# Optimization experiments

Measured on AMD Instinct MI355X. Metric: run time of the kernel, lower is better.

## Reference

```python
import jax, jax.numpy as jnp
import numpy as np

T_NUM = 1024      # tracks
DET_NUM = 1024    # detections
DEG = 64          # candidate detections per track
E = T_NUM * DEG   # directed track->det edges (row<col half)
N = T_NUM + DET_NUM
D_IN = 512
D_EMB = 256
LAM = 5.0
SLACK = -0.2
SINKHORN_ITERS = 8


def setup_inputs() -> dict:
    key = jax.random.key(0)
    ks = jax.random.split(key, 20)
    x = jax.random.normal(ks[0], (N, D_IN), jnp.float32)
    coords = jax.random.uniform(ks[1], (N, 4), dtype=jnp.float32)
    r = jax.random.uniform(ks[2], (N, 4), dtype=jnp.float32)
    bx1 = r[:, 0] * 100.0; by1 = r[:, 1] * 100.0
    bw = r[:, 2] * 50.0 + 1.0; bh = r[:, 3] * 50.0 + 1.0
    coords_original = jnp.stack([bx1, by1, bx1 + bw, by1 + bh], axis=1)
    src_t = jnp.repeat(jnp.arange(T_NUM, dtype=jnp.int32), DEG)
    off = jnp.tile(jnp.arange(DEG, dtype=jnp.int32), T_NUM)
    dst_d = (src_t * 13 + off) % DET_NUM            # unique det per (track, slot)
    src = src_t
    dst = dst_d + T_NUM                              # detection node ids come after tracks
    edge_index = jnp.concatenate([jnp.stack([src, dst]), jnp.stack([dst, src])], axis=1)
    ground_truth = jax.random.bernoulli(ks[3], 0.1, (T_NUM * DET_NUM,)).astype(jnp.float32)

    def lin(k, i, o):
        return jax.random.normal(k, (i, o), jnp.float32) / np.sqrt(i).astype(np.float32)

    params = {
        'W_enc': lin(ks[4], D_IN, D_EMB), 'b_enc': jnp.zeros((D_EMB,), jnp.float32),
        'W1a': lin(ks[5], 2 * D_EMB, 64), 'b1a': jnp.zeros((64,), jnp.float32),
        'W2a': lin(ks[6], 64, 1), 'b2a': jnp.zeros((1,), jnp.float32),
        'W1g': lin(ks[7], 8, 16), 'b1g': jnp.zeros((16,), jnp.float32),
        'W2g': lin(ks[8], 16, 1), 'b2g': jnp.zeros((1,), jnp.float32),
        'W1f': lin(ks[9], 2, 8), 'b1f': jnp.zeros((8,), jnp.float32),
        'W2f': lin(ks[10], 8, 1), 'b2f': jnp.zeros((1,), jnp.float32),
        'Wn': lin(ks[11], D_EMB, D_EMB), 'Wm': lin(ks[12], D_EMB, D_EMB),
        'bo': jnp.zeros((D_EMB,), jnp.float32),
        'W1c': lin(ks[13], 2, 8), 'b1c': jnp.zeros((8,), jnp.float32),
        'W2c': lin(ks[14], 8, 1), 'b2c': jnp.zeros((1,), jnp.float32),
    }
    out = {'x': x, 'coords': coords, 'coords_original': coords_original,
           'ground_truth': ground_truth, 'edge_index': edge_index}
    out.update(params)
    return out


def _box_iou(a, b):
    # a, b: [E, 4] boxes (x1, y1, x2, y2)
    lt = jnp.maximum(a[:, :2], b[:, :2])
    rb = jnp.minimum(a[:, 2:], b[:, 2:])
    wh = jnp.clip(rb - lt, 0.0)
    inter = wh[:, 0] * wh[:, 1]
    area_a = (a[:, 2] - a[:, 0]) * (a[:, 3] - a[:, 1])
    area_b = (b[:, 2] - b[:, 0]) * (b[:, 3] - b[:, 1])
    return inter / (area_a + area_b - inter + 1e-9)


def _sinkhorn(M):
    def body(M, _):
        M = M / (jnp.sum(M, axis=1, keepdims=True) + 1e-9)
        M = M / (jnp.sum(M, axis=0, keepdims=True) + 1e-9)
        return M, None
    M, _ = jax.lax.scan(body, M, None, length=SINKHORN_ITERS)
    return M


def _forward(x, coords, coords_original,
             W_enc, b_enc, W1a, b1a, W2a, b2a, W1g, b1g, W2g, b2g,
             W1f, b1f, W2f, b2f, Wn, Wm, bo, W1c, b1c, W2c, b2c,
             edge_index):
    node = jax.nn.relu(x @ W_enc + b_enc)                      # [N, D_EMB]
    src, dst = edge_index[0], edge_index[1]                    # [2E]
    # batched per-edge appearance affinity (replaces python edge loop)
    pair = jnp.concatenate([node[src], node[dst]], axis=1)     # [2E, 2*D_EMB]
    a1 = jax.nn.relu(pair @ W1a + b1a) @ W2a + b2a             # [2E, 1]
    geo = jnp.concatenate([coords[src], coords[dst]], axis=1)  # [2E, 8]
    a2 = jax.nn.relu(geo @ W1g + b1g) @ W2g + b2g              # [2E, 1]
    e_in = jnp.concatenate([a1, a2], axis=1)                   # [2E, 2]
    edge_emb = jax.nn.relu(e_in @ W1f + b1f) @ W2f + b2f       # [2E, 1]
    # optim_net: one round of edge-weighted message passing
    msg = jax.ops.segment_sum(edge_emb * node[src], dst, num_segments=N)
    out = jax.nn.relu(node @ Wn + msg @ Wm + bo)               # [N, D_EMB]
    # forward (row < col) edges are the first E entries by construction
    sf, df = src[:E], dst[:E]
    oa, ob = out[sf], out[df]
    denom = jnp.maximum(jnp.linalg.norm(oa, axis=1) * jnp.linalg.norm(ob, axis=1), 1e-6)
    cosv = jnp.sum(oa * ob, axis=1) / denom                    # CosineSimilarity(dim=0) per edge
    iou = _box_iou(coords_original[sf], coords_original[df])   # [E]
    f_in = jnp.stack([cosv, iou], axis=1)                      # [E, 2]
    aff = (jax.nn.relu(f_in @ W1c + b1c) @ W2c + b2c)[:, 0]    # [E]
    # assignment matrix with slack row/col, scatter exp(aff*lam)
    slack_val = jnp.exp(jnp.float32(SLACK * LAM))
    M = jnp.full((T_NUM + 1, DET_NUM + 1), slack_val, jnp.float32)
    M = M.at[:T_NUM, :DET_NUM].set(0.0)
    M = M.at[sf, df - T_NUM].set(jnp.exp(aff * LAM))
    M = _sinkhorn(M)
    return M[:-1, :-1].reshape(-1)                             # [T_NUM*DET_NUM]


def reference(x, coords, coords_original, ground_truth, edge_index,
              W_enc, b_enc, W1a, b1a, W2a, b2a, W1g, b1g, W2g, b2g,
              W1f, b1f, W2f, b2f, Wn, Wm, bo, W1c, b1c, W2c, b2c):
    normalized_output = _forward(x, coords, coords_original,
                                 W_enc, b_enc, W1a, b1a, W2a, b2a,
                                 W1g, b1g, W2g, b2g, W1f, b1f, W2f, b2f,
                                 Wn, Wm, bo, W1c, b1c, W2c, b2c, edge_index)
    det_num = jnp.asarray(DET_NUM, jnp.int32)
    tracklet_num = jnp.asarray(T_NUM, jnp.int32)
    return (normalized_output, ground_truth, det_num, tracklet_num)
```

## Files before the change

kernel.cpp:

```cpp
#include <hip/hip_runtime.h>

#define T_NUM 1024
#define DET_NUM 1024
#define E_NUM 65536
#define TWO_E 131072
#define N_NODES 2048
#define D_IN 512
#define D_EMB 256

__device__ __forceinline__ unsigned bf16r(float x) {
  const unsigned u = __float_as_uint(x);
  return (u + 0x7fffu + ((u >> 16) & 1u)) >> 16;
}
__device__ __forceinline__ float bflo(unsigned p) { return __uint_as_float(p << 16); }
__device__ __forceinline__ float bfhi(unsigned p) { return __uint_as_float(p & 0xffff0000u); }

__global__ __launch_bounds__(256) void k_enc_pg(
    const float* __restrict__ x, const float* __restrict__ W,
    const float* __restrict__ b, const float* __restrict__ coords,
    const float* __restrict__ W1a, const float* __restrict__ W1g,
    float* __restrict__ node, float* __restrict__ P1, float* __restrict__ P2,
    float* __restrict__ G1, float* __restrict__ G2) {
  __shared__ __align__(16) float ns[4][D_EMB];
  const int j = threadIdx.x;
  const int row0 = blockIdx.x * 4;
  float acc[4];
  const float bj = b[j];
#pragma unroll
  for (int r = 0; r < 4; r++) acc[r] = bj;
  const float* xr = x + (size_t)row0 * D_IN;
  for (int k = 0; k < D_IN; k += 4) {
    const float w0 = W[(k + 0) * D_EMB + j];
    const float w1 = W[(k + 1) * D_EMB + j];
    const float w2 = W[(k + 2) * D_EMB + j];
    const float w3 = W[(k + 3) * D_EMB + j];
#pragma unroll
    for (int r = 0; r < 4; r++) {
      const float4 xv = *reinterpret_cast<const float4*>(xr + (size_t)r * D_IN + k);
      acc[r] = fmaf(xv.x, w0, acc[r]);
      acc[r] = fmaf(xv.y, w1, acc[r]);
      acc[r] = fmaf(xv.z, w2, acc[r]);
      acc[r] = fmaf(xv.w, w3, acc[r]);
    }
  }
#pragma unroll
  for (int r = 0; r < 4; r++) {
    const float v = fmaxf(acc[r], 0.f);
    node[(size_t)(row0 + r) * D_EMB + j] = v;
    ns[r][j] = v;
  }
  __syncthreads();
  {
    const int r = j >> 6, h = j & 63;
    float a1 = 0.f, a2 = 0.f;
    for (int k = 0; k < D_EMB; k += 4) {
      const float4 nv = *reinterpret_cast<const float4*>(&ns[r][k]);
      a1 = fmaf(nv.x, W1a[(k + 0) * 64 + h], a1);
      a1 = fmaf(nv.y, W1a[(k + 1) * 64 + h], a1);
      a1 = fmaf(nv.z, W1a[(k + 2) * 64 + h], a1);
      a1 = fmaf(nv.w, W1a[(k + 3) * 64 + h], a1);
      a2 = fmaf(nv.x, W1a[(D_EMB + k + 0) * 64 + h], a2);
      a2 = fmaf(nv.y, W1a[(D_EMB + k + 1) * 64 + h], a2);
      a2 = fmaf(nv.z, W1a[(D_EMB + k + 2) * 64 + h], a2);
      a2 = fmaf(nv.w, W1a[(D_EMB + k + 3) * 64 + h], a2);
    }
    P1[(size_t)(row0 + r) * 64 + h] = a1;
    P2[(size_t)(row0 + r) * 64 + h] = a2;
  }
  if (j < 64) {
    const int r = j >> 4, h = j & 15;
    const int n = row0 + r;
    float g1 = 0.f, g2 = 0.f;
#pragma unroll
    for (int k = 0; k < 4; k++) {
      const float c = coords[(size_t)n * 4 + k];
      g1 = fmaf(c, W1g[k * 16 + h], g1);
      g2 = fmaf(c, W1g[(4 + k) * 16 + h], g2);
    }
    G1[(size_t)n * 16 + h] = g1;
    G2[(size_t)n * 16 + h] = g2;
  }
}

__global__ __launch_bounds__(256) void k_edge(
    const float* __restrict__ P1, const float* __restrict__ P2,
    const float* __restrict__ G1, const float* __restrict__ G2,
    const float* __restrict__ b1a, const float* __restrict__ W2a, const float* __restrict__ b2a,
    const float* __restrict__ b1g, const float* __restrict__ W2g, const float* __restrict__ b2g,
    const float* __restrict__ W1f, const float* __restrict__ b1f,
    const float* __restrict__ W2f, const float* __restrict__ b2f,
    float* __restrict__ wE) {
  const int e = blockIdx.x * 256 + threadIdx.x;
  int s, dn;
  if (e < E_NUM) {
    const int t = e >> 6, o = e & 63;
    s = t; dn = T_NUM + ((13 * t + o) & 1023);
  } else {
    const int e2 = e - E_NUM;
    const int t = e2 >> 6, o = e2 & 63;
    s = T_NUM + ((13 * t + o) & 1023); dn = t;
  }
  const float4* p1 = (const float4*)(P1 + (size_t)s * 64);
  const float4* p2 = (const float4*)(P2 + (size_t)dn * 64);
  const float4* b1 = (const float4*)b1a;
  const float4* w2 = (const float4*)W2a;
  float a1 = b2a[0];
#pragma unroll
  for (int i = 0; i < 16; i++) {
    const float4 pa = p1[i], pb = p2[i], bb = b1[i], ww = w2[i];
    a1 += fmaxf(pa.x + pb.x + bb.x, 0.f) * ww.x + fmaxf(pa.y + pb.y + bb.y, 0.f) * ww.y +
          fmaxf(pa.z + pb.z + bb.z, 0.f) * ww.z + fmaxf(pa.w + pb.w + bb.w, 0.f) * ww.w;
  }
  const float4* g1 = (const float4*)(G1 + (size_t)s * 16);
  const float4* g2 = (const float4*)(G2 + (size_t)dn * 16);
  const float4* bg = (const float4*)b1g;
  const float4* wg = (const float4*)W2g;
  float a2 = b2g[0];
#pragma unroll
  for (int i = 0; i < 4; i++) {
    const float4 pa = g1[i], pb = g2[i], bb = bg[i], ww = wg[i];
    a2 += fmaxf(pa.x + pb.x + bb.x, 0.f) * ww.x + fmaxf(pa.y + pb.y + bb.y, 0.f) * ww.y +
          fmaxf(pa.z + pb.z + bb.z, 0.f) * ww.z + fmaxf(pa.w + pb.w + bb.w, 0.f) * ww.w;
  }
  float acc = b2f[0];
#pragma unroll
  for (int jj = 0; jj < 8; jj++) {
    const float h = fmaxf(a1 * W1f[jj] + a2 * W1f[8 + jj] + b1f[jj], 0.f);
    acc = fmaf(h, W2f[jj], acc);
  }
  wE[e] = acc;
}

__global__ __launch_bounds__(256) void k_msg_out(
    const float* __restrict__ wE, const float* __restrict__ node,
    const float* __restrict__ Wn, const float* __restrict__ Wm,
    const float* __restrict__ bo, float* __restrict__ outE, float* __restrict__ nrm) {
  __shared__ __align__(16) float ms[4][D_EMB];
  __shared__ float wsh[4][64];
  __shared__ int ssh[4][64];
  __shared__ float redn[4][4];
  const int j = threadIdx.x;
  const int lane = j & 63, wid = j >> 6;
  const int row0 = blockIdx.x * 4;
  {
    const int r = j >> 6, o = j & 63;
    const int n = row0 + r;
    int e, src;
    if (n < T_NUM) {
      e = E_NUM + n * 64 + o;
      src = T_NUM + ((13 * n + o) & 1023);
    } else {
      const int d = n - T_NUM;
      const int t = (709 * (d - o)) & 1023;
      e = t * 64 + o;
      src = t;
    }
    wsh[r][o] = wE[e];
    ssh[r][o] = src;
  }
  __syncthreads();
#pragma unroll 1
  for (int r = 0; r < 4; r++) {
    float acc = 0.f;
#pragma unroll 4
    for (int i = 0; i < 64; i++)
      acc = fmaf(wsh[r][i], node[(size_t)ssh[r][i] * D_EMB + j], acc);
    ms[r][j] = acc;
  }
  __syncthreads();
  float acc[4];
  const float bj = bo[j];
#pragma unroll
  for (int r = 0; r < 4; r++) acc[r] = bj;
  const float* nrow = node + (size_t)row0 * D_EMB;
  for (int k = 0; k < D_EMB; k += 4) {
    const float wn0 = Wn[(k + 0) * D_EMB + j], wm0 = Wm[(k + 0) * D_EMB + j];
    const float wn1 = Wn[(k + 1) * D_EMB + j], wm1 = Wm[(k + 1) * D_EMB + j];
    const float wn2 = Wn[(k + 2) * D_EMB + j], wm2 = Wm[(k + 2) * D_EMB + j];
    const float wn3 = Wn[(k + 3) * D_EMB + j], wm3 = Wm[(k + 3) * D_EMB + j];
#pragma unroll
    for (int r = 0; r < 4; r++) {
      const float4 nv = *reinterpret_cast<const float4*>(nrow + (size_t)r * D_EMB + k);
      const float4 mv = *reinterpret_cast<const float4*>(&ms[r][k]);
      acc[r] = fmaf(nv.x, wn0, acc[r]); acc[r] = fmaf(mv.x, wm0, acc[r]);
      acc[r] = fmaf(nv.y, wn1, acc[r]); acc[r] = fmaf(mv.y, wm1, acc[r]);
      acc[r] = fmaf(nv.z, wn2, acc[r]); acc[r] = fmaf(mv.z, wm2, acc[r]);
      acc[r] = fmaf(nv.w, wn3, acc[r]); acc[r] = fmaf(mv.w, wm3, acc[r]);
    }
  }
#pragma unroll
  for (int r = 0; r < 4; r++) {
    acc[r] = fmaxf(acc[r], 0.f);
    outE[(size_t)(row0 + r) * D_EMB + j] = acc[r];
  }
#pragma unroll
  for (int r = 0; r < 4; r++) {
    float sq = acc[r] * acc[r];
#pragma unroll
    for (int o = 32; o > 0; o >>= 1) sq += __shfl_down(sq, o, 64);
    if (lane == 0) redn[wid][r] = sq;
  }
  __syncthreads();
  if (j < 4)
    nrm[row0 + j] = sqrtf(redn[0][j] + redn[1][j] + redn[2][j] + redn[3][j]);
}

__global__ __launch_bounds__(256) void k_aff(
    const float* __restrict__ outE, const float* __restrict__ nrm,
    const float* __restrict__ cov,
    const float* __restrict__ W1c, const float* __restrict__ b1c,
    const float* __restrict__ W2c, const float* __restrict__ b2c,
    float* __restrict__ Kbp, unsigned short* __restrict__ KTg) {
  const int e = blockIdx.x * 256 + threadIdx.x;
  const int t = e >> 6, o = e & 63;
  const int s = t;
  const int d = (13 * t + o) & 1023;
  const int dn = T_NUM + d;
  const float4* oa = (const float4*)(outE + (size_t)s * D_EMB);
  const float4* ob = (const float4*)(outE + (size_t)dn * D_EMB);
  float dot = 0.f;
#pragma unroll 8
  for (int i = 0; i < 64; i++) {
    const float4 a = oa[i], bq = ob[i];
    dot += a.x * bq.x + a.y * bq.y + a.z * bq.z + a.w * bq.w;
  }
  const float cosv = dot / fmaxf(nrm[s] * nrm[dn], 1e-6f);
  const float4 A = ((const float4*)cov)[s];
  const float4 B = ((const float4*)cov)[dn];
  const float ltx = fmaxf(A.x, B.x), lty = fmaxf(A.y, B.y);
  const float rbx = fminf(A.z, B.z), rby = fminf(A.w, B.w);
  const float wx = fmaxf(rbx - ltx, 0.f), wy = fmaxf(rby - lty, 0.f);
  const float inter = wx * wy;
  const float areaA = (A.z - A.x) * (A.w - A.y);
  const float areaB = (B.z - B.x) * (B.w - B.y);
  const float iou = inter / (areaA + areaB - inter + 1e-9f);
  float aff = b2c[0];
#pragma unroll
  for (int jj = 0; jj < 8; jj++) {
    const float h = fmaxf(cosv * W1c[jj] + iou * W1c[8 + jj] + b1c[jj], 0.f);
    aff = fmaf(h, W2c[jj], aff);
  }
  const float Kv = __expf(aff * 5.0f);
  const int tp = (13 * s) & 1023;
  Kbp[tp * 68 + (tp & 3) + o] = Kv;
  if (o < 4) {
    const int pr = (o < (tp & 3)) ? o : o + 64;
    Kbp[tp * 68 + pr] = 0.f;
  }
  const int cbase = (((d & 1022) + 960) & 1023) & ~3;
  const int rho = (((d + 961) & 1023) - cbase) & 1023;
  KTg[d * 72 + rho + 63 - o] = (unsigned short)bf16r(Kv);
  if (o < 8) {
    const int slot = (o < rho) ? o : o + 64;
    KTg[d * 72 + slot] = 0;
  }
}

__global__ __launch_bounds__(512, 2) void k_sinkhorn(
    const float* __restrict__ Kbp, const unsigned short* __restrict__ KTg,
    float* __restrict__ ug, float* __restrict__ vg) {
  __shared__ __align__(16) float u_lds[1092];
  __shared__ __align__(16) float v_lds[1092];
  __shared__ float red_u[8];
  __shared__ float red_v[8];
  const int tid = threadIdx.x;
  const int lane = tid & 63, wid = tid >> 6;
  const int ra = 2 * tid, rb = 2 * tid + 1;
  const int qa = (ra & ~3) >> 2;
  const int cbase = ((ra + 960) & 1023) & ~3;
  const int qc = cbase >> 2;
  unsigned k0[34], k1[34];
  {
    const float4* s0p = (const float4*)(Kbp + (size_t)ra * 68);
    const float4* s1p = (const float4*)(Kbp + (size_t)rb * 68);
#pragma unroll
    for (int c = 0; c < 17; c++) {
      float4 f = s0p[c];
      k0[2 * c]     = bf16r(f.x) | (bf16r(f.y) << 16);
      k0[2 * c + 1] = bf16r(f.z) | (bf16r(f.w) << 16);
      f = s1p[c];
      k1[2 * c]     = bf16r(f.x) | (bf16r(f.y) << 16);
      k1[2 * c + 1] = bf16r(f.z) | (bf16r(f.w) << 16);
    }
  }
  const uint4* kt0 = (const uint4*)(KTg + (size_t)ra * 72);
  const uint4* kt1 = (const uint4*)(KTg + (size_t)rb * 72);
  float u0 = 1.f, u1 = 1.f, vc0 = 1.f, vc1 = 1.f, u_sl = 1.f, v_sl = 1.f;
  v_lds[tid] = 1.f; v_lds[tid + 512] = 1.f;
  if (tid < 68) v_lds[1024 + tid] = 1.f;
  if (tid < 8) red_v[tid] = 128.f;
  const float slack = 0.36787944117144233f;
  __syncthreads();
#pragma unroll 1
  for (int it = 0; it < 8; ++it) {
    const float4* vq = (const float4*)v_lds;
    float a00 = 0.f, a01 = 0.f, a10 = 0.f, a11 = 0.f;
#pragma unroll
    for (int c = 0; c < 17; c++) {
      const float4 v4 = vq[qa + c];
      unsigned p = k0[2 * c];
      a00 = fmaf(bflo(p), v4.x, a00); a00 = fmaf(bfhi(p), v4.y, a00);
      p = k0[2 * c + 1];
      a01 = fmaf(bflo(p), v4.z, a01); a01 = fmaf(bfhi(p), v4.w, a01);
      p = k1[2 * c];
      a10 = fmaf(bflo(p), v4.x, a10); a10 = fmaf(bfhi(p), v4.y, a10);
      p = k1[2 * c + 1];
      a11 = fmaf(bflo(p), v4.z, a11); a11 = fmaf(bfhi(p), v4.w, a11);
    }
    const float sumv = red_v[0] + red_v[1] + red_v[2] + red_v[3] +
                       red_v[4] + red_v[5] + red_v[6] + red_v[7];
    const float s0 = a00 + a01 + slack * v_sl;
    const float s1 = a10 + a11 + slack * v_sl;
    u0 = u0 / (u0 * s0 + 1e-9f);
    u1 = u1 / (u1 * s1 + 1e-9f);
    u_sl = u_sl / (u_sl * slack * (sumv + v_sl) + 1e-9f);
    u_lds[ra] = u0; u_lds[rb] = u1;
    if (tid < 34) { u_lds[1024 + ra] = u0; u_lds[1024 + rb] = u1; }
    float usum = u0 + u1;
#pragma unroll
    for (int o = 32; o > 0; o >>= 1) usum += __shfl_down(usum, o, 64);
    if (lane == 0) red_u[wid] = usum;
    __syncthreads();
    const float4* uq = (const float4*)u_lds;
    float t0 = 0.f, t1 = 0.f;
#pragma unroll 3
    for (int q = 0; q < 9; q++) {
      const uint4 A = kt0[q];
      const uint4 B = kt1[q];
      const float4 ua = uq[qc + 2 * q];
      const float4 ub = uq[qc + 2 * q + 1];
      t0 = fmaf(bflo(A.x), ua.x, t0); t0 = fmaf(bfhi(A.x), ua.y, t0);
      t0 = fmaf(bflo(A.y), ua.z, t0); t0 = fmaf(bfhi(A.y), ua.w, t0);
      t0 = fmaf(bflo(A.z), ub.x, t0); t0 = fmaf(bfhi(A.z), ub.y, t0);
      t0 = fmaf(bflo(A.w), ub.z, t0); t0 = fmaf(bfhi(A.w), ub.w, t0);
      t1 = fmaf(bflo(B.x), ua.x, t1); t1 = fmaf(bfhi(B.x), ua.y, t1);
      t1 = fmaf(bflo(B.y), ua.z, t1); t1 = fmaf(bfhi(B.y), ua.w, t1);
      t1 = fmaf(bflo(B.z), ub.x, t1); t1 = fmaf(bfhi(B.z), ub.y, t1);
      t1 = fmaf(bflo(B.w), ub.z, t1); t1 = fmaf(bfhi(B.w), ub.w, t1);
    }
    const float sumu = red_u[0] + red_u[1] + red_u[2] + red_u[3] +
                       red_u[4] + red_u[5] + red_u[6] + red_u[7];
    t0 += slack * u_sl;
    t1 += slack * u_sl;
    vc0 = vc0 / (vc0 * t0 + 1e-9f);
    vc1 = vc1 / (vc1 * t1 + 1e-9f);
    v_sl = v_sl / (v_sl * slack * (sumu + u_sl) + 1e-9f);
    v_lds[ra] = vc0; v_lds[rb] = vc1;
    if (tid < 34) { v_lds[1024 + ra] = vc0; v_lds[1024 + rb] = vc1; }
    float vsum = vc0 + vc1;
#pragma unroll
    for (int o = 32; o > 0; o >>= 1) vsum += __shfl_down(vsum, o, 64);
    if (lane == 0) red_v[wid] = vsum;
    __syncthreads();
  }
  ((float2*)ug)[tid] = make_float2(u0, u1);
  ((float2*)vg)[tid] = make_float2(vc0, vc1);
}

__global__ __launch_bounds__(256) void k_final(
    const float* __restrict__ Kbp, const float* __restrict__ ug,
    const float* __restrict__ vg, const float* __restrict__ gt,
    float* __restrict__ out) {
  const int t = blockIdx.x;
  const int tp = (13 * t) & 1023;
  const float u = ug[tp];
  const float* krow = Kbp + (size_t)tp * 68 + (tp & 3);
  const int d0 = threadIdx.x * 4;
  const float4 v4 = ((const float4*)vg)[threadIdx.x];
  float4 o4;
  const int m0 = (d0 - tp) & 1023;
  const int m1 = (d0 + 1 - tp) & 1023;
  const int m2 = (d0 + 2 - tp) & 1023;
  const int m3 = (d0 + 3 - tp) & 1023;
  o4.x = (m0 < 64) ? u * krow[m0] * v4.x : 0.f;
  o4.y = (m1 < 64) ? u * krow[m1] * v4.y : 0.f;
  o4.z = (m2 < 64) ? u * krow[m2] * v4.z : 0.f;
  o4.w = (m3 < 64) ? u * krow[m3] * v4.w : 0.f;
  ((float4*)out)[(size_t)t * 256 + threadIdx.x] = o4;
  const float4 g4 = ((const float4*)gt)[(size_t)t * 256 + threadIdx.x];
  ((float4*)out)[(size_t)(T_NUM + t) * 256 + threadIdx.x] = g4;
  if (t == 0 && threadIdx.x == 0) {
    out[(size_t)2 * T_NUM * DET_NUM] = 1024.0f;
    out[(size_t)2 * T_NUM * DET_NUM + 1] = 1024.0f;
  }
}

extern "C" void kernel_launch(void* const* d_in, const int* in_sizes, int n_in,
                              void* d_out, int out_size, void* d_ws, size_t ws_size,
                              hipStream_t stream) {
  const float* x      = (const float*)d_in[0];
  const float* coords = (const float*)d_in[1];
  const float* cov    = (const float*)d_in[2];
  const float* gt     = (const float*)d_in[3];
  const float* W_enc  = (const float*)d_in[5];
  const float* b_enc  = (const float*)d_in[6];
  const float* W1a    = (const float*)d_in[7];
  const float* b1a    = (const float*)d_in[8];
  const float* W2a    = (const float*)d_in[9];
  const float* b2a    = (const float*)d_in[10];
  const float* W1g    = (const float*)d_in[11];
  const float* b1g    = (const float*)d_in[12];
  const float* W2g    = (const float*)d_in[13];
  const float* b2g    = (const float*)d_in[14];
  const float* W1f    = (const float*)d_in[15];
  const float* b1f    = (const float*)d_in[16];
  const float* W2f    = (const float*)d_in[17];
  const float* b2f    = (const float*)d_in[18];
  const float* Wn     = (const float*)d_in[19];
  const float* Wm     = (const float*)d_in[20];
  const float* bo     = (const float*)d_in[21];
  const float* W1c    = (const float*)d_in[22];
  const float* b1c    = (const float*)d_in[23];
  const float* W2c    = (const float*)d_in[24];
  const float* b2c    = (const float*)d_in[25];

  char* ws = (char*)d_ws;
  size_t off = 0;
  auto alloc = [&](size_t bytes) {
    char* p = ws + off;
    off = (off + bytes + 255) & ~(size_t)255;
    return p;
  };
  float* node  = (float*)alloc((size_t)N_NODES * D_EMB * 4);
  float* P1    = (float*)alloc((size_t)N_NODES * 64 * 4);
  float* P2    = (float*)alloc((size_t)N_NODES * 64 * 4);
  float* G1    = (float*)alloc((size_t)N_NODES * 16 * 4);
  float* G2    = (float*)alloc((size_t)N_NODES * 16 * 4);
  float* wE    = (float*)alloc((size_t)TWO_E * 4);
  float* outE  = (float*)alloc((size_t)N_NODES * D_EMB * 4);
  float* nrm   = (float*)alloc((size_t)N_NODES * 4);
  float* Kbp   = (float*)alloc((size_t)1024 * 68 * 4);
  unsigned short* KTg = (unsigned short*)alloc((size_t)1024 * 72 * 2);
  float* ug    = (float*)alloc(1024 * 4);
  float* vg    = (float*)alloc(1024 * 4);
  float* out   = (float*)d_out;

  k_enc_pg<<<N_NODES / 4, 256, 0, stream>>>(x, W_enc, b_enc, coords, W1a, W1g,
                                            node, P1, P2, G1, G2);
  k_edge<<<TWO_E / 256, 256, 0, stream>>>(P1, P2, G1, G2, b1a, W2a, b2a,
                                          b1g, W2g, b2g, W1f, b1f, W2f, b2f, wE);
  k_msg_out<<<N_NODES / 4, 256, 0, stream>>>(wE, node, Wn, Wm, bo, outE, nrm);
  k_aff<<<E_NUM / 256, 256, 0, stream>>>(outE, nrm, cov, W1c, b1c, W2c, b2c,
                                         Kbp, KTg);
  k_sinkhorn<<<1, 512, 0, stream>>>(Kbp, KTg, ug, vg);
  k_final<<<T_NUM, 256, 0, stream>>>(Kbp, ug, vg, gt, out);
}
```

Measured before the change: 242.1 us.

## Split encoder K-dimension across two half-blocks and widen single-block Sinkhorn to 1024 threads

The encoder kernel now uses 512 threads per block handling 8 rows. Each half of the block computes a partial dot product over half of D_IN, and the halves are combined through shared memory, which doubles per-block work and the reuse of W loads. The single-block Sinkhorn kernel now runs 1024 threads with one row and one column per thread. It also keeps the transposed K slice in registers instead of re-reading global memory every iteration, to shorten the serial critical path. In exchange it adds an extra barrier in the encoder, raises register pressure, and spreads the Sinkhorn reduction over 16 waves.

```diff
diff --git a/kernel.cpp b/kernel.cpp
--- a/kernel.cpp
+++ b/kernel.cpp
@@ -15,27 +15,31 @@
 __device__ __forceinline__ float bflo(unsigned p) { return __uint_as_float(p << 16); }
 __device__ __forceinline__ float bfhi(unsigned p) { return __uint_as_float(p & 0xffff0000u); }
 
-__global__ __launch_bounds__(256) void k_enc_pg(
+__global__ __launch_bounds__(512) void k_enc_pg(
     const float* __restrict__ x, const float* __restrict__ W,
     const float* __restrict__ b, const float* __restrict__ coords,
     const float* __restrict__ W1a, const float* __restrict__ W1g,
     float* __restrict__ node, float* __restrict__ P1, float* __restrict__ P2,
     float* __restrict__ G1, float* __restrict__ G2) {
-  __shared__ __align__(16) float ns[4][D_EMB];
-  const int j = threadIdx.x;
-  const int row0 = blockIdx.x * 4;
-  float acc[4];
+  __shared__ __align__(16) float ns[8][D_EMB];
+  __shared__ __align__(16) float ps[8][D_EMB];
+  const int tid = threadIdx.x;
+  const int j = tid & 255;
+  const int h = __builtin_amdgcn_readfirstlane(tid >> 8);
+  const int row0 = blockIdx.x * 8;
+  float acc[8];
   const float bj = b[j];
 #pragma unroll
-  for (int r = 0; r < 4; r++) acc[r] = bj;
-  const float* xr = x + (size_t)row0 * D_IN;
-  for (int k = 0; k < D_IN; k += 4) {
-    const float w0 = W[(k + 0) * D_EMB + j];
-    const float w1 = W[(k + 1) * D_EMB + j];
-    const float w2 = W[(k + 2) * D_EMB + j];
-    const float w3 = W[(k + 3) * D_EMB + j];
-#pragma unroll
-    for (int r = 0; r < 4; r++) {
+  for (int r = 0; r < 8; r++) acc[r] = (h == 0) ? bj : 0.f;
+  const float* xr = x + (size_t)row0 * D_IN + h * 256;
+  const float* Wp = W + (size_t)h * 256 * D_EMB;
+  for (int k = 0; k < 256; k += 4) {
+    const float w0 = Wp[(k + 0) * D_EMB + j];
+    const float w1 = Wp[(k + 1) * D_EMB + j];
+    const float w2 = Wp[(k + 2) * D_EMB + j];
+    const float w3 = Wp[(k + 3) * D_EMB + j];
+#pragma unroll
+    for (int r = 0; r < 8; r++) {
       const float4 xv = *reinterpret_cast<const float4*>(xr + (size_t)r * D_IN + k);
       acc[r] = fmaf(xv.x, w0, acc[r]);
       acc[r] = fmaf(xv.y, w1, acc[r]);
@@ -43,42 +47,49 @@
       acc[r] = fmaf(xv.w, w3, acc[r]);
     }
   }
-#pragma unroll
-  for (int r = 0; r < 4; r++) {
-    const float v = fmaxf(acc[r], 0.f);
-    node[(size_t)(row0 + r) * D_EMB + j] = v;
-    ns[r][j] = v;
+  if (h == 1) {
+#pragma unroll
+    for (int r = 0; r < 8; r++) ps[r][j] = acc[r];
+  }
+  __syncthreads();
+  if (h == 0) {
+#pragma unroll
+    for (int r = 0; r < 8; r++) {
+      const float v = fmaxf(acc[r] + ps[r][j], 0.f);
+      node[(size_t)(row0 + r) * D_EMB + j] = v;
+      ns[r][j] = v;
+    }
   }
   __syncthreads();
   {
-    const int r = j >> 6, h = j & 63;
+    const int r = tid >> 6, hh = tid & 63;
     float a1 = 0.f, a2 = 0.f;
     for (int k = 0; k < D_EMB; k += 4) {
       const float4 nv = *reinterpret_cast<const float4*>(&ns[r][k]);
-      a1 = fmaf(nv.x, W1a[(k + 0) * 64 + h], a1);
-      a1 = fmaf(nv.y, W1a[(k + 1) * 64 + h], a1);
-      a1 = fmaf(nv.z, W1a[(k + 2) * 64 + h], a1);
-      a1 = fmaf(nv.w, W1a[(k + 3) * 64 + h], a1);
-      a2 = fmaf(nv.x, W1a[(D_EMB + k + 0) * 64 + h], a2);
-      a2 = fmaf(nv.y, W1a[(D_EMB + k + 1) * 64 + h], a2);
-      a2 = fmaf(nv.z, W1a[(D_EMB + k + 2) * 64 + h], a2);
-      a2 = fmaf(nv.w, W1a[(D_EMB + k + 3) * 64 + h], a2);
-    }
-    P1[(size_t)(row0 + r) * 64 + h] = a1;
-    P2[(size_t)(row0 + r) * 64 + h] = a2;
-  }
-  if (j < 64) {
-    const int r = j >> 4, h = j & 15;
+      a1 = fmaf(nv.x, W1a[(k + 0) * 64 + hh], a1);
+      a1 = fmaf(nv.y, W1a[(k + 1) * 64 + hh], a1);
+      a1 = fmaf(nv.z, W1a[(k + 2) * 64 + hh], a1);
+      a1 = fmaf(nv.w, W1a[(k + 3) * 64 + hh], a1);
+      a2 = fmaf(nv.x, W1a[(D_EMB + k + 0) * 64 + hh], a2);
+      a2 = fmaf(nv.y, W1a[(D_EMB + k + 1) * 64 + hh], a2);
+      a2 = fmaf(nv.z, W1a[(D_EMB + k + 2) * 64 + hh], a2);
+      a2 = fmaf(nv.w, W1a[(D_EMB + k + 3) * 64 + hh], a2);
+    }
+    P1[(size_t)(row0 + r) * 64 + hh] = a1;
+    P2[(size_t)(row0 + r) * 64 + hh] = a2;
+  }
+  if (tid < 128) {
+    const int r = tid >> 4, hh = tid & 15;
     const int n = row0 + r;
     float g1 = 0.f, g2 = 0.f;
 #pragma unroll
     for (int k = 0; k < 4; k++) {
       const float c = coords[(size_t)n * 4 + k];
-      g1 = fmaf(c, W1g[k * 16 + h], g1);
-      g2 = fmaf(c, W1g[(4 + k) * 16 + h], g2);
-    }
-    G1[(size_t)n * 16 + h] = g1;
-    G2[(size_t)n * 16 + h] = g2;
+      g1 = fmaf(c, W1g[k * 16 + hh], g1);
+      g2 = fmaf(c, W1g[(4 + k) * 16 + hh], g2);
+    }
+    G1[(size_t)n * 16 + hh] = g1;
+    G2[(size_t)n * 16 + hh] = g2;
   }
 }
 
@@ -256,105 +267,92 @@
   }
 }
 
-__global__ __launch_bounds__(512, 2) void k_sinkhorn(
+__global__ __launch_bounds__(1024, 4) void k_sinkhorn(
     const float* __restrict__ Kbp, const unsigned short* __restrict__ KTg,
     float* __restrict__ ug, float* __restrict__ vg) {
   __shared__ __align__(16) float u_lds[1092];
   __shared__ __align__(16) float v_lds[1092];
-  __shared__ float red_u[8];
-  __shared__ float red_v[8];
+  __shared__ float red_u[16];
+  __shared__ float red_v[16];
   const int tid = threadIdx.x;
   const int lane = tid & 63, wid = tid >> 6;
-  const int ra = 2 * tid, rb = 2 * tid + 1;
-  const int qa = (ra & ~3) >> 2;
-  const int cbase = ((ra + 960) & 1023) & ~3;
-  const int qc = cbase >> 2;
-  unsigned k0[34], k1[34];
+  unsigned kr[34];
   {
-    const float4* s0p = (const float4*)(Kbp + (size_t)ra * 68);
-    const float4* s1p = (const float4*)(Kbp + (size_t)rb * 68);
+    const float4* sp = (const float4*)(Kbp + (size_t)tid * 68);
 #pragma unroll
     for (int c = 0; c < 17; c++) {
-      float4 f = s0p[c];
-      k0[2 * c]     = bf16r(f.x) | (bf16r(f.y) << 16);
-      k0[2 * c + 1] = bf16r(f.z) | (bf16r(f.w) << 16);
-      f = s1p[c];
-      k1[2 * c]     = bf16r(f.x) | (bf16r(f.y) << 16);
-      k1[2 * c + 1] = bf16r(f.z) | (bf16r(f.w) << 16);
-    }
-  }
-  const uint4* kt0 = (const uint4*)(KTg + (size_t)ra * 72);
-  const uint4* kt1 = (const uint4*)(KTg + (size_t)rb * 72);
-  float u0 = 1.f, u1 = 1.f, vc0 = 1.f, vc1 = 1.f, u_sl = 1.f, v_sl = 1.f;
-  v_lds[tid] = 1.f; v_lds[tid + 512] = 1.f;
+      const float4 f = sp[c];
+      kr[2 * c]     = bf16r(f.x) | (bf16r(f.y) << 16);
+      kr[2 * c + 1] = bf16r(f.z) | (bf16r(f.w) << 16);
+    }
+  }
+  uint4 kt[9];
+  {
+    const uint4* kp = (const uint4*)(KTg + (size_t)tid * 72);
+#pragma unroll
+    for (int q = 0; q < 9; q++) kt[q] = kp[q];
+  }
+  const int qa = tid & ~3;
+  const int cb = (((tid & ~1) + 960) & 1023) & ~3;
+  float u = 1.f, v = 1.f, u_sl = 1.f, v_sl = 1.f;
+  v_lds[tid] = 1.f;
   if (tid < 68) v_lds[1024 + tid] = 1.f;
-  if (tid < 8) red_v[tid] = 128.f;
+  if (tid < 16) red_v[tid] = 64.f;
   const float slack = 0.36787944117144233f;
   __syncthreads();
 #pragma unroll 1
   for (int it = 0; it < 8; ++it) {
-    const float4* vq = (const float4*)v_lds;
-    float a00 = 0.f, a01 = 0.f, a10 = 0.f, a11 = 0.f;
+    const float4* vq = (const float4*)(v_lds + qa);
+    float a0 = 0.f, a1 = 0.f;
 #pragma unroll
     for (int c = 0; c < 17; c++) {
-      const float4 v4 = vq[qa + c];
-      unsigned p = k0[2 * c];
-      a00 = fmaf(bflo(p), v4.x, a00); a00 = fmaf(bfhi(p), v4.y, a00);
-      p = k0[2 * c + 1];
-      a01 = fmaf(bflo(p), v4.z, a01); a01 = fmaf(bfhi(p), v4.w, a01);
-      p = k1[2 * c];
-      a10 = fmaf(bflo(p), v4.x, a10); a10 = fmaf(bfhi(p), v4.y, a10);
-      p = k1[2 * c + 1];
-      a11 = fmaf(bflo(p), v4.z, a11); a11 = fmaf(bfhi(p), v4.w, a11);
-    }
-    const float sumv = red_v[0] + red_v[1] + red_v[2] + red_v[3] +
-                       red_v[4] + red_v[5] + red_v[6] + red_v[7];
-    const float s0 = a00 + a01 + slack * v_sl;
-    const float s1 = a10 + a11 + slack * v_sl;
-    u0 = u0 / (u0 * s0 + 1e-9f);
-    u1 = u1 / (u1 * s1 + 1e-9f);
+      const float4 v4 = vq[c];
+      unsigned p = kr[2 * c];
+      a0 = fmaf(bflo(p), v4.x, a0); a0 = fmaf(bfhi(p), v4.y, a0);
+      p = kr[2 * c + 1];
+      a1 = fmaf(bflo(p), v4.z, a1); a1 = fmaf(bfhi(p), v4.w, a1);
+    }
+    float sumv = 0.f;
+#pragma unroll
+    for (int i = 0; i < 16; i++) sumv += red_v[i];
+    const float s = a0 + a1 + slack * v_sl;
+    u = u / (u * s + 1e-9f);
     u_sl = u_sl / (u_sl * slack * (sumv + v_sl) + 1e-9f);
-    u_lds[ra] = u0; u_lds[rb] = u1;
-    if (tid < 34) { u_lds[1024 + ra] = u0; u_lds[1024 + rb] = u1; }
-    float usum = u0 + u1;
+    u_lds[tid] = u;
+    if (tid < 68) u_lds[1024 + tid] = u;
+    float usum = u;
 #pragma unroll
     for (int o = 32; o > 0; o >>= 1) usum += __shfl_down(usum, o, 64);
     if (lane == 0) red_u[wid] = usum;
     __syncthreads();
-    const float4* uq = (const float4*)u_lds;
+    const float4* uq = (const float4*)(u_lds + cb);
     float t0 = 0.f, t1 = 0.f;
-#pragma unroll 3
+#pragma unroll
     for (int q = 0; q < 9; q++) {
-      const uint4 A = kt0[q];
-      const uint4 B = kt1[q];
-      const float4 ua = uq[qc + 2 * q];
-      const float4 ub = uq[qc + 2 * q + 1];
+      const uint4 A = kt[q];
+      const float4 ua = uq[2 * q];
+      const float4 ub = uq[2 * q + 1];
       t0 = fmaf(bflo(A.x), ua.x, t0); t0 = fmaf(bfhi(A.x), ua.y, t0);
       t0 = fmaf(bflo(A.y), ua.z, t0); t0 = fmaf(bfhi(A.y), ua.w, t0);
-      t0 = fmaf(bflo(A.z), ub.x, t0); t0 = fmaf(bfhi(A.z), ub.y, t0);
-      t0 = fmaf(bflo(A.w), ub.z, t0); t0 = fmaf(bfhi(A.w), ub.w, t0);
-      t1 = fmaf(bflo(B.x), ua.x, t1); t1 = fmaf(bfhi(B.x), ua.y, t1);
-      t1 = fmaf(bflo(B.y), ua.z, t1); t1 = fmaf(bfhi(B.y), ua.w, t1);
-      t1 = fmaf(bflo(B.z), ub.x, t1); t1 = fmaf(bfhi(B.z), ub.y, t1);
-      t1 = fmaf(bflo(B.w), ub.z, t1); t1 = fmaf(bfhi(B.w), ub.w, t1);
-    }
-    const float sumu = red_u[0] + red_u[1] + red_u[2] + red_u[3] +
-                       red_u[4] + red_u[5] + red_u[6] + red_u[7];
-    t0 += slack * u_sl;
-    t1 += slack * u_sl;
-    vc0 = vc0 / (vc0 * t0 + 1e-9f);
-    vc1 = vc1 / (vc1 * t1 + 1e-9f);
+      t1 = fmaf(bflo(A.z), ub.x, t1); t1 = fmaf(bfhi(A.z), ub.y, t1);
+      t1 = fmaf(bflo(A.w), ub.z, t1); t1 = fmaf(bfhi(A.w), ub.w, t1);
+    }
+    float sumu = 0.f;
+#pragma unroll
+    for (int i = 0; i < 16; i++) sumu += red_u[i];
+    const float tv = t0 + t1 + slack * u_sl;
+    v = v / (v * tv + 1e-9f);
     v_sl = v_sl / (v_sl * slack * (sumu + u_sl) + 1e-9f);
-    v_lds[ra] = vc0; v_lds[rb] = vc1;
-    if (tid < 34) { v_lds[1024 + ra] = vc0; v_lds[1024 + rb] = vc1; }
-    float vsum = vc0 + vc1;
+    v_lds[tid] = v;
+    if (tid < 68) v_lds[1024 + tid] = v;
+    float vsum = v;
 #pragma unroll
     for (int o = 32; o > 0; o >>= 1) vsum += __shfl_down(vsum, o, 64);
     if (lane == 0) red_v[wid] = vsum;
     __syncthreads();
   }
-  ((float2*)ug)[tid] = make_float2(u0, u1);
-  ((float2*)vg)[tid] = make_float2(vc0, vc1);
+  ug[tid] = u;
+  vg[tid] = v;
 }
 
 __global__ __launch_bounds__(256) void k_final(
@@ -435,13 +433,13 @@
   float* vg    = (float*)alloc(1024 * 4);
   float* out   = (float*)d_out;
 
-  k_enc_pg<<<N_NODES / 4, 256, 0, stream>>>(x, W_enc, b_enc, coords, W1a, W1g,
+  k_enc_pg<<<N_NODES / 8, 512, 0, stream>>>(x, W_enc, b_enc, coords, W1a, W1g,
                                             node, P1, P2, G1, G2);
   k_edge<<<TWO_E / 256, 256, 0, stream>>>(P1, P2, G1, G2, b1a, W2a, b2a,
                                           b1g, W2g, b2g, W1f, b1f, W2f, b2f, wE);
   k_msg_out<<<N_NODES / 4, 256, 0, stream>>>(wE, node, Wn, Wm, bo, outE, nrm);
   k_aff<<<E_NUM / 256, 256, 0, stream>>>(outE, nrm, cov, W1c, b1c, W2c, b2c,
                                          Kbp, KTg);
-  k_sinkhorn<<<1, 512, 0, stream>>>(Kbp, KTg, ug, vg);
+  k_sinkhorn<<<1, 1024, 0, stream>>>(Kbp, KTg, ug, vg);
   k_final<<<T_NUM, 256, 0, stream>>>(Kbp, ug, vg, gt, out);
 }
```

New measurement: 278.6 us. 1.15x slower.

## Split encoder K across two half-blocks and stage sinkhorn KT tiles in LDS

Applied to the files above, without the earlier changes.

The encoder kernel now handles 8 rows per block with 512 threads. The two halves split the 512-wide input dimension, and partial sums are combined through shared memory, so each weight load feeds twice as many rows. The single-block sinkhorn kernel copies its transposed bf16 kernel slices into LDS once, so each of the 8 iterations reads them from LDS instead of global/L2. The cost is about 147KB of LDS in the sinkhorn kernel and an extra barrier plus reduction in the encoder.

```diff
diff --git a/kernel.cpp b/kernel.cpp
--- a/kernel.cpp
+++ b/kernel.cpp
@@ -15,27 +15,31 @@
 __device__ __forceinline__ float bflo(unsigned p) { return __uint_as_float(p << 16); }
 __device__ __forceinline__ float bfhi(unsigned p) { return __uint_as_float(p & 0xffff0000u); }
 
-__global__ __launch_bounds__(256) void k_enc_pg(
+__global__ __launch_bounds__(512) void k_enc_pg(
     const float* __restrict__ x, const float* __restrict__ W,
     const float* __restrict__ b, const float* __restrict__ coords,
     const float* __restrict__ W1a, const float* __restrict__ W1g,
     float* __restrict__ node, float* __restrict__ P1, float* __restrict__ P2,
     float* __restrict__ G1, float* __restrict__ G2) {
-  __shared__ __align__(16) float ns[4][D_EMB];
-  const int j = threadIdx.x;
-  const int row0 = blockIdx.x * 4;
-  float acc[4];
+  __shared__ __align__(16) float ns[8][D_EMB];
+  __shared__ __align__(16) float ps[8][D_EMB];
+  const int tid = threadIdx.x;
+  const int j = tid & 255;
+  const int h = __builtin_amdgcn_readfirstlane(tid >> 8);
+  const int row0 = blockIdx.x * 8;
+  float acc[8];
   const float bj = b[j];
 #pragma unroll
-  for (int r = 0; r < 4; r++) acc[r] = bj;
-  const float* xr = x + (size_t)row0 * D_IN;
-  for (int k = 0; k < D_IN; k += 4) {
-    const float w0 = W[(k + 0) * D_EMB + j];
-    const float w1 = W[(k + 1) * D_EMB + j];
-    const float w2 = W[(k + 2) * D_EMB + j];
-    const float w3 = W[(k + 3) * D_EMB + j];
-#pragma unroll
-    for (int r = 0; r < 4; r++) {
+  for (int r = 0; r < 8; r++) acc[r] = (h == 0) ? bj : 0.f;
+  const float* xr = x + (size_t)row0 * D_IN + h * 256;
+  const float* Wp = W + (size_t)h * 256 * D_EMB;
+  for (int k = 0; k < 256; k += 4) {
+    const float w0 = Wp[(k + 0) * D_EMB + j];
+    const float w1 = Wp[(k + 1) * D_EMB + j];
+    const float w2 = Wp[(k + 2) * D_EMB + j];
+    const float w3 = Wp[(k + 3) * D_EMB + j];
+#pragma unroll
+    for (int r = 0; r < 8; r++) {
       const float4 xv = *reinterpret_cast<const float4*>(xr + (size_t)r * D_IN + k);
       acc[r] = fmaf(xv.x, w0, acc[r]);
       acc[r] = fmaf(xv.y, w1, acc[r]);
@@ -43,42 +47,49 @@
       acc[r] = fmaf(xv.w, w3, acc[r]);
     }
   }
-#pragma unroll
-  for (int r = 0; r < 4; r++) {
-    const float v = fmaxf(acc[r], 0.f);
-    node[(size_t)(row0 + r) * D_EMB + j] = v;
-    ns[r][j] = v;
+  if (h == 1) {
+#pragma unroll
+    for (int r = 0; r < 8; r++) ps[r][j] = acc[r];
+  }
+  __syncthreads();
+  if (h == 0) {
+#pragma unroll
+    for (int r = 0; r < 8; r++) {
+      const float v = fmaxf(acc[r] + ps[r][j], 0.f);
+      node[(size_t)(row0 + r) * D_EMB + j] = v;
+      ns[r][j] = v;
+    }
   }
   __syncthreads();
   {
-    const int r = j >> 6, h = j & 63;
+    const int r = tid >> 6, hh = tid & 63;
     float a1 = 0.f, a2 = 0.f;
     for (int k = 0; k < D_EMB; k += 4) {
       const float4 nv = *reinterpret_cast<const float4*>(&ns[r][k]);
-      a1 = fmaf(nv.x, W1a[(k + 0) * 64 + h], a1);
-      a1 = fmaf(nv.y, W1a[(k + 1) * 64 + h], a1);
-      a1 = fmaf(nv.z, W1a[(k + 2) * 64 + h], a1);
-      a1 = fmaf(nv.w, W1a[(k + 3) * 64 + h], a1);
-      a2 = fmaf(nv.x, W1a[(D_EMB + k + 0) * 64 + h], a2);
-      a2 = fmaf(nv.y, W1a[(D_EMB + k + 1) * 64 + h], a2);
-      a2 = fmaf(nv.z, W1a[(D_EMB + k + 2) * 64 + h], a2);
-      a2 = fmaf(nv.w, W1a[(D_EMB + k + 3) * 64 + h], a2);
-    }
-    P1[(size_t)(row0 + r) * 64 + h] = a1;
-    P2[(size_t)(row0 + r) * 64 + h] = a2;
-  }
-  if (j < 64) {
-    const int r = j >> 4, h = j & 15;
+      a1 = fmaf(nv.x, W1a[(k + 0) * 64 + hh], a1);
+      a1 = fmaf(nv.y, W1a[(k + 1) * 64 + hh], a1);
+      a1 = fmaf(nv.z, W1a[(k + 2) * 64 + hh], a1);
+      a1 = fmaf(nv.w, W1a[(k + 3) * 64 + hh], a1);
+      a2 = fmaf(nv.x, W1a[(D_EMB + k + 0) * 64 + hh], a2);
+      a2 = fmaf(nv.y, W1a[(D_EMB + k + 1) * 64 + hh], a2);
+      a2 = fmaf(nv.z, W1a[(D_EMB + k + 2) * 64 + hh], a2);
+      a2 = fmaf(nv.w, W1a[(D_EMB + k + 3) * 64 + hh], a2);
+    }
+    P1[(size_t)(row0 + r) * 64 + hh] = a1;
+    P2[(size_t)(row0 + r) * 64 + hh] = a2;
+  }
+  if (tid < 128) {
+    const int r = tid >> 4, hh = tid & 15;
     const int n = row0 + r;
     float g1 = 0.f, g2 = 0.f;
 #pragma unroll
     for (int k = 0; k < 4; k++) {
       const float c = coords[(size_t)n * 4 + k];
-      g1 = fmaf(c, W1g[k * 16 + h], g1);
-      g2 = fmaf(c, W1g[(4 + k) * 16 + h], g2);
-    }
-    G1[(size_t)n * 16 + h] = g1;
-    G2[(size_t)n * 16 + h] = g2;
+      g1 = fmaf(c, W1g[k * 16 + hh], g1);
+      g2 = fmaf(c, W1g[(4 + k) * 16 + hh], g2);
+    }
+    G1[(size_t)n * 16 + hh] = g1;
+    G2[(size_t)n * 16 + hh] = g2;
   }
 }
 
@@ -263,6 +274,8 @@
   __shared__ __align__(16) float v_lds[1092];
   __shared__ float red_u[8];
   __shared__ float red_v[8];
+  __shared__ __align__(16) uint4 ktlA[9][512];
+  __shared__ __align__(16) uint4 ktlB[9][512];
   const int tid = threadIdx.x;
   const int lane = tid & 63, wid = tid >> 6;
   const int ra = 2 * tid, rb = 2 * tid + 1;
@@ -283,8 +296,13 @@
       k1[2 * c + 1] = bf16r(f.z) | (bf16r(f.w) << 16);
     }
   }
-  const uint4* kt0 = (const uint4*)(KTg + (size_t)ra * 72);
-  const uint4* kt1 = (const uint4*)(KTg + (size_t)rb * 72);
+  {
+    const uint4* g = (const uint4*)KTg;
+#pragma unroll
+    for (int q = 0; q < 9; q++) ktlA[q][tid] = g[tid * 18 + q];
+#pragma unroll
+    for (int q = 0; q < 9; q++) ktlB[q][tid] = g[tid * 18 + 9 + q];
+  }
   float u0 = 1.f, u1 = 1.f, vc0 = 1.f, vc1 = 1.f, u_sl = 1.f, v_sl = 1.f;
   v_lds[tid] = 1.f; v_lds[tid + 512] = 1.f;
   if (tid < 68) v_lds[1024 + tid] = 1.f;
@@ -325,8 +343,8 @@
     float t0 = 0.f, t1 = 0.f;
 #pragma unroll 3
     for (int q = 0; q < 9; q++) {
-      const uint4 A = kt0[q];
-      const uint4 B = kt1[q];
+      const uint4 A = ktlA[q][tid];
+      const uint4 B = ktlB[q][tid];
       const float4 ua = uq[qc + 2 * q];
       const float4 ub = uq[qc + 2 * q + 1];
       t0 = fmaf(bflo(A.x), ua.x, t0); t0 = fmaf(bfhi(A.x), ua.y, t0);
@@ -435,7 +453,7 @@
   float* vg    = (float*)alloc(1024 * 4);
   float* out   = (float*)d_out;
 
-  k_enc_pg<<<N_NODES / 4, 256, 0, stream>>>(x, W_enc, b_enc, coords, W1a, W1g,
+  k_enc_pg<<<N_NODES / 8, 512, 0, stream>>>(x, W_enc, b_enc, coords, W1a, W1g,
                                             node, P1, P2, G1, G2);
   k_edge<<<TWO_E / 256, 256, 0, stream>>>(P1, P2, G1, G2, b1a, W2a, b2a,
                                           b1g, W2g, b2g, W1f, b1f, W2f, b2f, wE);
```

After: 221.9 us. -8.3%, faster.
